# Kernel tuning notes

Measured on AMD Instinct MI355X. Metric: run time of the kernel, lower is better.

## Reference

```python
import jax, jax.numpy as jnp
import numpy as np

B, N, D, E, H, F, L = 4096, 32, 128, 256, 8, 1024, 6
DH = E // H  # head dim = 32
LN_EPS = 1e-5


def setup_inputs() -> dict:
    key = jax.random.key(0)
    ks = jax.random.split(key, 8)
    def s(k, shape, fan_in):
        return (jax.random.normal(k, shape, jnp.float32) / np.float32(np.sqrt(fan_in)))
    inp = {
        "obs": jax.random.normal(ks[0], (B, D), jnp.float32),
        "emb_W": s(ks[1], (N, D, E), D),          # per-node tokenizer Linear weights
        "emb_b": jnp.zeros((N, E), jnp.float32),
        "pos_emb": jax.random.normal(ks[2], (N, E), jnp.float32) * 0.02,
        "Wqkv": s(ks[3], (3 * E, E), E),          # shared across all L layers (torch code shares one layer object)
        "bqkv": jnp.zeros((3 * E,), jnp.float32),
        "Wo": s(ks[4], (E, E), E),
        "bo": jnp.zeros((E,), jnp.float32),
        "ln1_g": jnp.ones((E,), jnp.float32),
        "ln1_b": jnp.zeros((E,), jnp.float32),
        "ln2_g": jnp.ones((E,), jnp.float32),
        "ln2_b": jnp.zeros((E,), jnp.float32),
        "W1": s(ks[5], (E, F), E),
        "b1": jnp.zeros((F,), jnp.float32),
        "W2": s(ks[6], (F, E), F),
        "b2": jnp.zeros((E,), jnp.float32),
    }
    # kinematic-chain adjacency (|i-j|<=1) incl. forced self-loops, additive mask
    idx = jnp.arange(N)
    adj = jnp.abs(idx[:, None] - idx[None, :]) <= 1
    inp["adj_mask"] = jnp.where(adj, 0.0, -1e9).astype(jnp.float32)  # [N, N]
    return inp


def _layer_norm(x, g, b):
    m = jnp.mean(x, axis=-1, keepdims=True)
    v = jnp.var(x, axis=-1, keepdims=True)
    return (x - m) * jax.lax.rsqrt(v + LN_EPS) * g + b


def _encoder_layer(x, adj_mask, Wqkv, bqkv, Wo, bo, ln1_g, ln1_b, ln2_g, ln2_b, W1, b1, W2, b2):
    # pre-LN self-attention block
    h = _layer_norm(x, ln1_g, ln1_b)                      # [B, N, E]
    qkv = h @ Wqkv.T + bqkv                               # [B, N, 3E]
    q, k, v = jnp.split(qkv, 3, axis=-1)
    q = q.reshape(B, N, H, DH).transpose(0, 2, 1, 3)      # [B, H, N, DH]
    k = k.reshape(B, N, H, DH).transpose(0, 2, 1, 3)
    v = v.reshape(B, N, H, DH).transpose(0, 2, 1, 3)
    scale = np.float32(1.0 / np.sqrt(DH))
    scores = jnp.einsum('bhqd,bhkd->bhqk', q, k) * scale + adj_mask  # [B, H, N, N]
    attn = jax.nn.softmax(scores, axis=-1)
    o = jnp.einsum('bhqk,bhkd->bhqd', attn, v)
    o = o.transpose(0, 2, 1, 3).reshape(B, N, E)
    x = x + (o @ Wo.T + bo)
    # pre-LN feed-forward block (ReLU)
    h2 = _layer_norm(x, ln2_g, ln2_b)
    x = x + (jax.nn.relu(h2 @ W1 + b1) @ W2 + b2)
    return x


def reference(obs, emb_W, emb_b, pos_emb, Wqkv, bqkv, Wo, bo,
              ln1_g, ln1_b, ln2_g, ln2_b, W1, b1, W2, b2, adj_mask):
    # per-node MLP tokenizer (every node sees full obs): [B,D] x [N,D,E] -> [B,N,E]
    x = jnp.einsum('bd,nde->bne', obs, emb_W) + emb_b + pos_emb
    # BoT-Hard: all L layers masked; torch ModuleList shares a single layer's params
    for _ in range(L):
        x = _encoder_layer(x, adj_mask, Wqkv, bqkv, Wo, bo,
                           ln1_g, ln1_b, ln2_g, ln2_b, W1, b1, W2, b2)
    return x
```

## Files before the change

kernel.cpp:

```cpp
#include <hip/hip_runtime.h>
#include <hip/hip_bf16.h>
#include <stdint.h>

#define B_ 4096
#define N_ 32
#define D_ 128
#define E_ 256
#define H_ 8
#define F_ 1024
#define L_ 6
#define M_ (B_ * N_)

typedef unsigned short u16;
typedef __attribute__((ext_vector_type(8))) short short8;
typedef __attribute__((ext_vector_type(4))) short short4v;
typedef __attribute__((ext_vector_type(4))) float floatx4;

__device__ __forceinline__ float b2f(u16 u) {
  union { unsigned int i; float f; } c;
  c.i = ((unsigned int)u) << 16;
  return c.f;
}
__device__ __forceinline__ u16 f2b(float f) {
  union { float f; unsigned int i; } c;
  c.f = f;
  unsigned int x = c.i;
  return (u16)((x + 0x7fffu + ((x >> 16) & 1u)) >> 16);
}

typedef __attribute__((address_space(1))) void* gas_ptr;
typedef __attribute__((address_space(3))) void* las_ptr;
__device__ __forceinline__ void async16(const u16* g, u16* l) {
  __builtin_amdgcn_global_load_lds((gas_ptr)g, (las_ptr)l, 16, 0, 0);
}

template <bool RELU>
__global__ __launch_bounds__(256) void gemm_async(
    const u16* __restrict__ A, int lda,
    const u16* __restrict__ Bt,
    const float* __restrict__ bias,
    u16* __restrict__ C, int ldc,
    int K) {
  __shared__ u16 As[128 * 32];
  __shared__ u16 Bs[128 * 32];
  const int tid = threadIdx.x;
  const int wave = tid >> 6;
  const int lane = tid & 63;
  const int wm = wave & 1;
  const int wn = wave >> 1;
  const int lrow = lane & 15;
  const int quad = lane >> 4;
  const long m0 = (long)blockIdx.x * 128;
  const long n0 = (long)blockIdx.y * 128;

  const u16* Ab = A + m0 * lda;
  const u16* Bb = Bt + n0 * K;

  floatx4 acc[4][4];
#pragma unroll
  for (int a = 0; a < 4; ++a)
#pragma unroll
    for (int b = 0; b < 4; ++b) acc[a][b] = floatx4{0.f, 0.f, 0.f, 0.f};

  const int rr = tid >> 2;
  const int oo = (tid & 3) * 8;
  u16* lA0 = As + wave * 512;
  u16* lA1 = As + 2048 + wave * 512;
  u16* lB0 = Bs + wave * 512;
  u16* lB1 = Bs + 2048 + wave * 512;

  for (int kb = 0; kb < K; kb += 32) {
    __syncthreads();
    async16(Ab + (long)rr * lda + kb + oo, lA0);
    async16(Ab + (long)(rr + 64) * lda + kb + oo, lA1);
    async16(Bb + (long)rr * K + kb + oo, lB0);
    async16(Bb + (long)(rr + 64) * K + kb + oo, lB1);
    __syncthreads();
    short8 af[4], bfr[4];
#pragma unroll
    for (int t = 0; t < 4; ++t) {
      af[t] = *(const short8*)(As + (wm * 64 + t * 16 + lrow) * 32 + quad * 8);
      bfr[t] = *(const short8*)(Bs + (wn * 64 + t * 16 + lrow) * 32 + quad * 8);
    }
#pragma unroll
    for (int tm = 0; tm < 4; ++tm)
#pragma unroll
      for (int tn = 0; tn < 4; ++tn)
        acc[tm][tn] = __builtin_amdgcn_mfma_f32_16x16x32_bf16(af[tm], bfr[tn], acc[tm][tn], 0, 0, 0);
  }

#pragma unroll
  for (int tn = 0; tn < 4; ++tn) {
    const long col = n0 + wn * 64 + tn * 16 + lrow;
    const float bv = bias[col];
#pragma unroll
    for (int tm = 0; tm < 4; ++tm) {
#pragma unroll
      for (int r = 0; r < 4; ++r) {
        const long row = m0 + wm * 64 + tm * 16 + quad * 4 + r;
        float v = acc[tm][tn][r] + bv;
        if (RELU) v = fmaxf(v, 0.0f);
        C[row * (long)ldc + col] = f2b(v);
      }
    }
  }
}

template <bool RESID>
__global__ __launch_bounds__(512) void gemm_ln(
    const u16* __restrict__ A, int lda, long sAz,
    const u16* __restrict__ Bt, long sBz,
    const float* __restrict__ bias, long sBiasz,
    float* __restrict__ xout, u16* __restrict__ hout,
    int ldc, long sCz,
    const float* __restrict__ resid,
    const float* __restrict__ g, const float* __restrict__ be,
    int K) {
  __shared__ u16 As[128 * 32];
  __shared__ u16 Bs[256 * 32];
  __shared__ float part[128][4][2];
  const int tid = threadIdx.x;
  const int wave = tid >> 6;
  const int lane = tid & 63;
  const int wm = wave >> 2;
  const int wn = wave & 3;
  const int lrow = lane & 15;
  const int quad = lane >> 4;
  const int z = blockIdx.z;
  const long m0 = (long)blockIdx.x * 128;

  const u16* Ab = A + (long)z * sAz + m0 * lda;
  const u16* Bb = Bt + (long)z * sBz;

  floatx4 acc[4][4];
#pragma unroll
  for (int a = 0; a < 4; ++a)
#pragma unroll
    for (int b = 0; b < 4; ++b) acc[a][b] = floatx4{0.f, 0.f, 0.f, 0.f};

  const int rr = tid >> 2;
  const int oo = (tid & 3) * 8;
  u16* lA = As + wave * 512;
  u16* lB0 = Bs + wave * 512;
  u16* lB1 = Bs + 4096 + wave * 512;

  for (int kb = 0; kb < K; kb += 32) {
    __syncthreads();
    async16(Ab + (long)rr * lda + kb + oo, lA);
    async16(Bb + (long)rr * K + kb + oo, lB0);
    async16(Bb + (long)(rr + 128) * K + kb + oo, lB1);
    __syncthreads();
    short8 af[4], bfr[4];
#pragma unroll
    for (int t = 0; t < 4; ++t) {
      af[t] = *(const short8*)(As + (wm * 64 + t * 16 + lrow) * 32 + quad * 8);
      bfr[t] = *(const short8*)(Bs + (wn * 64 + t * 16 + lrow) * 32 + quad * 8);
    }
#pragma unroll
    for (int tm = 0; tm < 4; ++tm)
#pragma unroll
      for (int tn = 0; tn < 4; ++tn)
        acc[tm][tn] = __builtin_amdgcn_mfma_f32_16x16x32_bf16(af[tm], bfr[tn], acc[tm][tn], 0, 0, 0);
  }

  const long cz = (long)z * sCz;
  float bv[4];
#pragma unroll
  for (int tn = 0; tn < 4; ++tn)
    bv[tn] = bias[(long)z * sBiasz + wn * 64 + tn * 16 + lrow];
#pragma unroll
  for (int tm = 0; tm < 4; ++tm) {
#pragma unroll
    for (int r = 0; r < 4; ++r) {
      const long row = m0 + wm * 64 + tm * 16 + quad * 4 + r;
#pragma unroll
      for (int tn = 0; tn < 4; ++tn) {
        float v = acc[tm][tn][r] + bv[tn];
        if (RESID) {
          const long col = wn * 64 + tn * 16 + lrow;
          v += resid[cz + row * (long)ldc + col];
        }
        acc[tm][tn][r] = v;
      }
    }
  }

#pragma unroll
  for (int tm = 0; tm < 4; ++tm) {
#pragma unroll
    for (int r = 0; r < 4; ++r) {
      float s = acc[tm][0][r] + acc[tm][1][r] + acc[tm][2][r] + acc[tm][3][r];
      float q = acc[tm][0][r] * acc[tm][0][r] + acc[tm][1][r] * acc[tm][1][r] +
                acc[tm][2][r] * acc[tm][2][r] + acc[tm][3][r] * acc[tm][3][r];
#pragma unroll
      for (int mk = 1; mk <= 8; mk <<= 1) {
        s += __shfl_xor(s, mk, 64);
        q += __shfl_xor(q, mk, 64);
      }
      if (lrow == 0) {
        const int lr = wm * 64 + tm * 16 + quad * 4 + r;
        part[lr][wn][0] = s;
        part[lr][wn][1] = q;
      }
    }
  }
  __syncthreads();

  float gv[4], bev[4];
#pragma unroll
  for (int tn = 0; tn < 4; ++tn) {
    const int col = wn * 64 + tn * 16 + lrow;
    gv[tn] = g[col];
    bev[tn] = be[col];
  }
#pragma unroll
  for (int tm = 0; tm < 4; ++tm) {
#pragma unroll
    for (int r = 0; r < 4; ++r) {
      const int lr = wm * 64 + tm * 16 + quad * 4 + r;
      const float s = part[lr][0][0] + part[lr][1][0] + part[lr][2][0] + part[lr][3][0];
      const float q = part[lr][0][1] + part[lr][1][1] + part[lr][2][1] + part[lr][3][1];
      const float mean = s * (1.0f / 256.0f);
      const float var = q * (1.0f / 256.0f) - mean * mean;
      const float rstd = rsqrtf(var + 1e-5f);
      const long row = m0 + lr;
#pragma unroll
      for (int tn = 0; tn < 4; ++tn) {
        const int col = wn * 64 + tn * 16 + lrow;
        const long idx = cz + row * (long)ldc + col;
        const float v = acc[tm][tn][r];
        xout[idx] = v;
        hout[idx] = f2b((v - mean) * rstd * gv[tn] + bev[tn]);
      }
    }
  }
}

__global__ __launch_bounds__(256) void attn_kernel(const u16* __restrict__ qkv,
                                                   u16* __restrict__ o) {
  const int t = blockIdx.x * 256 + threadIdx.x;
  const int i = t & 31;
  const int h = (t >> 5) & 7;
  const long b = (long)(t >> 8);
  const long m = b * 32 + i;
  const u16* qp = qkv + m * 768 + h * 32;
  float q[32];
#pragma unroll
  for (int c = 0; c < 4; ++c) {
    short8 qv = *(const short8*)(qp + c * 8);
#pragma unroll
    for (int k = 0; k < 8; ++k) q[c * 8 + k] = b2f((u16)qv[k]);
  }
  float sc[3];
  int jc[3];
#pragma unroll
  for (int jj = 0; jj < 3; ++jj) {
    const int j = i - 1 + jj;
    const bool valid = (j >= 0) && (j < 32);
    const int jcl = valid ? j : i;
    jc[jj] = jcl;
    const u16* kp = qkv + (b * 32 + jcl) * 768 + 256 + h * 32;
    float dot = 0.0f;
#pragma unroll
    for (int c = 0; c < 4; ++c) {
      short8 kv = *(const short8*)(kp + c * 8);
#pragma unroll
      for (int k = 0; k < 8; ++k) dot += q[c * 8 + k] * b2f((u16)kv[k]);
    }
    sc[jj] = valid ? dot * 0.17677669529663687f : -3.0e38f;
  }
  const float mx = fmaxf(sc[0], fmaxf(sc[1], sc[2]));
  const float w0 = __expf(sc[0] - mx);
  const float w1 = __expf(sc[1] - mx);
  const float w2 = __expf(sc[2] - mx);
  const float inv = 1.0f / (w0 + w1 + w2);
  const float w[3] = {w0 * inv, w1 * inv, w2 * inv};
  float acc[32];
#pragma unroll
  for (int k = 0; k < 32; ++k) acc[k] = 0.0f;
#pragma unroll
  for (int jj = 0; jj < 3; ++jj) {
    const u16* vp = qkv + (b * 32 + jc[jj]) * 768 + 512 + h * 32;
    const float wj = w[jj];
#pragma unroll
    for (int c = 0; c < 4; ++c) {
      short8 vv = *(const short8*)(vp + c * 8);
#pragma unroll
      for (int k = 0; k < 8; ++k) acc[c * 8 + k] += wj * b2f((u16)vv[k]);
    }
  }
  u16* op = o + m * 256 + h * 32;
#pragma unroll
  for (int c = 0; c < 4; ++c) {
    short8 ov;
#pragma unroll
    for (int k = 0; k < 8; ++k) ov[k] = (short)f2b(acc[c * 8 + k]);
    *(short8*)(op + c * 8) = ov;
  }
}

__global__ __launch_bounds__(256) void transpose_f2b(const float* __restrict__ src,
                                                     u16* __restrict__ dst,
                                                     int R, int C) {
  const long base = (long)blockIdx.z * R * C;
  const int idx = blockIdx.x * 256 + threadIdx.x;
  if (idx < R * C) {
    const int r = idx / C;
    const int c = idx - r * C;
    dst[base + (long)c * R + r] = f2b(src[base + idx]);
  }
}

__global__ __launch_bounds__(256) void cvt_f2b_kernel(const float* __restrict__ s,
                                                      u16* __restrict__ d, int n) {
  const int i = blockIdx.x * 256 + threadIdx.x;
  if (i < n) d[i] = f2b(s[i]);
}

__global__ __launch_bounds__(256) void addf_kernel(const float* __restrict__ a,
                                                   const float* __restrict__ b,
                                                   float* __restrict__ d, int n) {
  const int i = blockIdx.x * 256 + threadIdx.x;
  if (i < n) d[i] = a[i] + b[i];
}

extern "C" void kernel_launch(void* const* d_in, const int* in_sizes, int n_in,
                              void* d_out, int out_size, void* d_ws, size_t ws_size,
                              hipStream_t stream) {
  (void)in_sizes; (void)n_in; (void)out_size; (void)ws_size;
  const float* obs   = (const float*)d_in[0];
  const float* emb_W = (const float*)d_in[1];
  const float* emb_b = (const float*)d_in[2];
  const float* pos   = (const float*)d_in[3];
  const float* Wqkv  = (const float*)d_in[4];
  const float* bqkv  = (const float*)d_in[5];
  const float* Wo    = (const float*)d_in[6];
  const float* bo    = (const float*)d_in[7];
  const float* ln1_g = (const float*)d_in[8];
  const float* ln1_b = (const float*)d_in[9];
  const float* ln2_g = (const float*)d_in[10];
  const float* ln2_b = (const float*)d_in[11];
  const float* W1    = (const float*)d_in[12];
  const float* b1    = (const float*)d_in[13];
  const float* W2    = (const float*)d_in[14];
  const float* b2    = (const float*)d_in[15];

  float* x = (float*)d_out;

  char* ws = (char*)d_ws;
  u16* hbuf   = (u16*)ws;   ws += (size_t)M_ * E_ * 2;
  u16* sbuf   = (u16*)ws;   ws += (size_t)M_ * F_ * 2;
  u16* embWt  = (u16*)ws;   ws += (size_t)N_ * D_ * E_ * 2;
  u16* obs_bf = (u16*)ws;   ws += (size_t)B_ * D_ * 2;
  u16* wqkv_bf= (u16*)ws;   ws += (size_t)3 * E_ * E_ * 2;
  u16* wo_bf  = (u16*)ws;   ws += (size_t)E_ * E_ * 2;
  u16* w1t    = (u16*)ws;   ws += (size_t)E_ * F_ * 2;
  u16* w2t    = (u16*)ws;   ws += (size_t)E_ * F_ * 2;
  float* cbias= (float*)ws; ws += (size_t)N_ * E_ * 4;

  transpose_f2b<<<dim3((D_ * E_ + 255) / 256, 1, N_), 256, 0, stream>>>(emb_W, embWt, D_, E_);
  transpose_f2b<<<dim3((E_ * F_ + 255) / 256, 1, 1), 256, 0, stream>>>(W1, w1t, E_, F_);
  transpose_f2b<<<dim3((E_ * F_ + 255) / 256, 1, 1), 256, 0, stream>>>(W2, w2t, F_, E_);
  cvt_f2b_kernel<<<(B_ * D_ + 255) / 256, 256, 0, stream>>>(obs, obs_bf, B_ * D_);
  cvt_f2b_kernel<<<(3 * E_ * E_ + 255) / 256, 256, 0, stream>>>(Wqkv, wqkv_bf, 3 * E_ * E_);
  cvt_f2b_kernel<<<(E_ * E_ + 255) / 256, 256, 0, stream>>>(Wo, wo_bf, E_ * E_);
  addf_kernel<<<(N_ * E_ + 255) / 256, 256, 0, stream>>>(emb_b, pos, cbias, N_ * E_);

  gemm_ln<false><<<dim3(B_ / 128, 1, N_), 512, 0, stream>>>(
      obs_bf, D_, 0, embWt, (long)E_ * D_, cbias, E_,
      x, hbuf, N_ * E_, E_, nullptr, ln1_g, ln1_b, D_);

  for (int l = 0; l < L_; ++l) {
    gemm_async<false><<<dim3(M_ / 128, 768 / 128, 1), 256, 0, stream>>>(
        hbuf, E_, wqkv_bf, bqkv, sbuf, 768, E_);
    attn_kernel<<<(M_ * H_) / 256, 256, 0, stream>>>(sbuf, hbuf);
    gemm_ln<true><<<dim3(M_ / 128, 1, 1), 512, 0, stream>>>(
        hbuf, E_, 0, wo_bf, 0, bo, 0,
        x, hbuf, E_, 0, x, ln2_g, ln2_b, E_);
    gemm_async<true><<<dim3(M_ / 128, F_ / 128, 1), 256, 0, stream>>>(
        hbuf, E_, w1t, b1, sbuf, F_, E_);
    gemm_ln<true><<<dim3(M_ / 128, 1, 1), 512, 0, stream>>>(
        sbuf, F_, 0, w2t, 0, b2, 0,
        x, hbuf, E_, 0, x, ln1_g, ln1_b, F_);
  }
}
```

Before: 4.266 ms.

## Double-buffer LDS tiles in both GEMM kernels to overlap loads with MFMA

Both GEMM kernels now keep two LDS buffers per operand and prefetch the next K-slice with async global-to-LDS loads while the current slice is consumed by MFMA. Raw s_barrier plus explicit vmcnt waits replace the two __syncthreads per iteration, which previously fully serialized load and compute. This doubles the LDS footprint per block, which may reduce occupancy. Correctness relies on the vmcnt counts matching the number of outstanding loads issued per thread.

```diff
diff --git a/kernel.cpp b/kernel.cpp
--- a/kernel.cpp
+++ b/kernel.cpp
@@ -34,6 +34,9 @@
   __builtin_amdgcn_global_load_lds((gas_ptr)g, (las_ptr)l, 16, 0, 0);
 }
 
+#define RAW_BARRIER() __builtin_amdgcn_s_barrier()
+#define WAITV(n) asm volatile("s_waitcnt vmcnt(" #n ")" ::: "memory")
+
 template <bool RELU>
 __global__ __launch_bounds__(256) void gemm_async(
     const u16* __restrict__ A, int lda,
@@ -41,8 +44,8 @@
     const float* __restrict__ bias,
     u16* __restrict__ C, int ldc,
     int K) {
-  __shared__ u16 As[128 * 32];
-  __shared__ u16 Bs[128 * 32];
+  __shared__ u16 As[2][128 * 32];
+  __shared__ u16 Bs[2][128 * 32];
   const int tid = threadIdx.x;
   const int wave = tid >> 6;
   const int lane = tid & 63;
@@ -64,23 +67,34 @@
 
   const int rr = tid >> 2;
   const int oo = (tid & 3) * 8;
-  u16* lA0 = As + wave * 512;
-  u16* lA1 = As + 2048 + wave * 512;
-  u16* lB0 = Bs + wave * 512;
-  u16* lB1 = Bs + 2048 + wave * 512;
-
-  for (int kb = 0; kb < K; kb += 32) {
-    __syncthreads();
-    async16(Ab + (long)rr * lda + kb + oo, lA0);
-    async16(Ab + (long)(rr + 64) * lda + kb + oo, lA1);
-    async16(Bb + (long)rr * K + kb + oo, lB0);
-    async16(Bb + (long)(rr + 64) * K + kb + oo, lB1);
-    __syncthreads();
+
+#define ISSUE_GA(p, kb)                                              \
+  do {                                                               \
+    async16(Ab + (long)rr * lda + (kb) + oo, &As[p][wave * 512]);    \
+    async16(Ab + (long)(rr + 64) * lda + (kb) + oo,                  \
+            &As[p][2048 + wave * 512]);                              \
+    async16(Bb + (long)rr * K + (kb) + oo, &Bs[p][wave * 512]);      \
+    async16(Bb + (long)(rr + 64) * K + (kb) + oo,                    \
+            &Bs[p][2048 + wave * 512]);                              \
+  } while (0)
+
+  const int T = K >> 5;
+  ISSUE_GA(0, 0);
+  for (int i = 0; i < T; ++i) {
+    const int cur = i & 1;
+    RAW_BARRIER();
+    if (i + 1 < T) {
+      ISSUE_GA(cur ^ 1, (i + 1) * 32);
+      WAITV(4);
+    } else {
+      WAITV(0);
+    }
+    RAW_BARRIER();
     short8 af[4], bfr[4];
 #pragma unroll
     for (int t = 0; t < 4; ++t) {
-      af[t] = *(const short8*)(As + (wm * 64 + t * 16 + lrow) * 32 + quad * 8);
-      bfr[t] = *(const short8*)(Bs + (wn * 64 + t * 16 + lrow) * 32 + quad * 8);
+      af[t] = *(const short8*)(&As[cur][(wm * 64 + t * 16 + lrow) * 32 + quad * 8]);
+      bfr[t] = *(const short8*)(&Bs[cur][(wn * 64 + t * 16 + lrow) * 32 + quad * 8]);
     }
 #pragma unroll
     for (int tm = 0; tm < 4; ++tm)
@@ -88,6 +102,7 @@
       for (int tn = 0; tn < 4; ++tn)
         acc[tm][tn] = __builtin_amdgcn_mfma_f32_16x16x32_bf16(af[tm], bfr[tn], acc[tm][tn], 0, 0, 0);
   }
+#undef ISSUE_GA
 
 #pragma unroll
   for (int tn = 0; tn < 4; ++tn) {
@@ -116,8 +131,8 @@
     const float* __restrict__ resid,
     const float* __restrict__ g, const float* __restrict__ be,
     int K) {
-  __shared__ u16 As[128 * 32];
-  __shared__ u16 Bs[256 * 32];
+  __shared__ u16 As[2][128 * 32];
+  __shared__ u16 Bs[2][256 * 32];
   __shared__ float part[128][4][2];
   const int tid = threadIdx.x;
   const int wave = tid >> 6;
@@ -140,21 +155,32 @@
 
   const int rr = tid >> 2;
   const int oo = (tid & 3) * 8;
-  u16* lA = As + wave * 512;
-  u16* lB0 = Bs + wave * 512;
-  u16* lB1 = Bs + 4096 + wave * 512;
-
-  for (int kb = 0; kb < K; kb += 32) {
-    __syncthreads();
-    async16(Ab + (long)rr * lda + kb + oo, lA);
-    async16(Bb + (long)rr * K + kb + oo, lB0);
-    async16(Bb + (long)(rr + 128) * K + kb + oo, lB1);
-    __syncthreads();
+
+#define ISSUE_GL(p, kb)                                               \
+  do {                                                                \
+    async16(Ab + (long)rr * lda + (kb) + oo, &As[p][wave * 512]);     \
+    async16(Bb + (long)rr * K + (kb) + oo, &Bs[p][wave * 512]);       \
+    async16(Bb + (long)(rr + 128) * K + (kb) + oo,                    \
+            &Bs[p][4096 + wave * 512]);                               \
+  } while (0)
+
+  const int T = K >> 5;
+  ISSUE_GL(0, 0);
+  for (int i = 0; i < T; ++i) {
+    const int cur = i & 1;
+    RAW_BARRIER();
+    if (i + 1 < T) {
+      ISSUE_GL(cur ^ 1, (i + 1) * 32);
+      WAITV(3);
+    } else {
+      WAITV(0);
+    }
+    RAW_BARRIER();
     short8 af[4], bfr[4];
 #pragma unroll
     for (int t = 0; t < 4; ++t) {
-      af[t] = *(const short8*)(As + (wm * 64 + t * 16 + lrow) * 32 + quad * 8);
-      bfr[t] = *(const short8*)(Bs + (wn * 64 + t * 16 + lrow) * 32 + quad * 8);
+      af[t] = *(const short8*)(&As[cur][(wm * 64 + t * 16 + lrow) * 32 + quad * 8]);
+      bfr[t] = *(const short8*)(&Bs[cur][(wn * 64 + t * 16 + lrow) * 32 + quad * 8]);
     }
 #pragma unroll
     for (int tm = 0; tm < 4; ++tm)
@@ -162,6 +188,7 @@
       for (int tn = 0; tn < 4; ++tn)
         acc[tm][tn] = __builtin_amdgcn_mfma_f32_16x16x32_bf16(af[tm], bfr[tn], acc[tm][tn], 0, 0, 0);
   }
+#undef ISSUE_GL
 
   const long cz = (long)z * sCz;
   float bv[4];
```

Measured after the change: 4.221 ms. About the same (-1.0%).
